# Optimization experiments

Hardware: AMD Instinct MI355X
Metric: run time of the kernel (lower is better)

The kernel has to match this reference:

```python
import jax, jax.numpy as jnp
import numpy as np

BATCH = 32
NUM_PRIORS = 8732
NUM_CLASSES = 81          # includes background class 0
CENTER_VAR = 0.1
SIZE_VAR = 0.2
CONF_THR = 0.01
NMS_THR = 0.45
TOPK = 100                # per-class NMS candidates
MAX_DET = 100             # max detections per image


def setup_inputs() -> dict:
    key = jax.random.key(0)
    k1, k2, k3 = jax.random.split(key, 3)
    cls_logits = jax.random.normal(k1, (BATCH, NUM_PRIORS, NUM_CLASSES), jnp.float32)
    bbox_pred = jax.random.normal(k2, (BATCH, NUM_PRIORS, 4), jnp.float32)
    # center-form priors (cx, cy, w, h) in (0, 1)
    priors = jax.random.uniform(k3, (NUM_PRIORS, 4), jnp.float32, 0.05, 0.95)
    return {"cls_logits": cls_logits, "bbox_pred": bbox_pred, "priors": priors}


def _decode(loc, priors):
    # convert_locations_to_boxes (center form) then center_form_to_corner_form
    cxcy = loc[..., :2] * CENTER_VAR * priors[..., 2:] + priors[..., :2]
    wh = jnp.exp(loc[..., 2:] * SIZE_VAR) * priors[..., 2:]
    return jnp.concatenate([cxcy - wh * 0.5, cxcy + wh * 0.5], axis=-1)  # [.., 4] xyxy


def _pairwise_iou(b):
    # b: [K, 4] corner form
    lt = jnp.maximum(b[:, None, :2], b[None, :, :2])
    rb = jnp.minimum(b[:, None, 2:], b[None, :, 2:])
    wh = jnp.clip(rb - lt, 0.0)
    inter = wh[..., 0] * wh[..., 1]
    area = jnp.clip(b[:, 2] - b[:, 0], 0.0) * jnp.clip(b[:, 3] - b[:, 1], 0.0)
    return inter / (area[:, None] + area[None, :] - inter + 1e-9)


def _per_class_nms(scores_n, boxes_n):
    # scores_n: [N], boxes_n: [N, 4]
    s, idx = jax.lax.top_k(scores_n, TOPK)
    b = boxes_n[idx]                                # [K, 4]
    iou = _pairwise_iou(b)                          # [K, K]
    init = s > CONF_THR
    rng = jnp.arange(TOPK)

    def body(i, keep):
        sup = (iou[i] > NMS_THR) & keep[i] & (rng > i)
        return keep & ~sup

    keep = jax.lax.fori_loop(0, TOPK, body, init)   # greedy NMS on sorted boxes
    return jnp.where(keep, s, 0.0), b


def reference(cls_logits, bbox_pred, priors):
    scores = jax.nn.softmax(cls_logits, axis=-1)            # [B, N, C]
    boxes = _decode(bbox_pred, priors)                      # [B, N, 4]
    cls_scores = jnp.swapaxes(scores[..., 1:], 1, 2)        # [B, C-1, N] skip background
    nms_fn = jax.vmap(jax.vmap(_per_class_nms, in_axes=(0, None)), in_axes=(0, 0))
    s_k, b_k = nms_fn(cls_scores, boxes)                    # [B, C-1, K], [B, C-1, K, 4]
    labels = jnp.broadcast_to(jnp.arange(1, NUM_CLASSES)[None, :, None], s_k.shape)
    B = s_k.shape[0]
    flat = (NUM_CLASSES - 1) * TOPK
    s_f = s_k.reshape(B, flat)
    b_f = b_k.reshape(B, flat, 4)
    l_f = labels.reshape(B, flat)
    top_s, top_i = jax.lax.top_k(s_f, MAX_DET)              # keep best MAX_DET per image
    top_b = jnp.take_along_axis(b_f, top_i[..., None], axis=1)
    top_l = jnp.take_along_axis(l_f, top_i, axis=1)
    return top_b, top_s, top_l.astype(jnp.int32)
```

## Files before the change

### kernel.cpp

```cpp
#include <hip/hip_runtime.h>
#include <hip/hip_bf16.h>
#include <float.h>

#define BATCH    32
#define NPRIORS  8732
#define NT       137
#define NPAD     (NT * 64)
#define NV4T     (NPAD / 4)
#define NCLASSES 81
#define NC1      80
#define TOPK     100
#define MAXDET   100
#define FLATC    (NC1 * TOPK)
#define FV4      2000
#define NCAND    512
#define NBIN     1024
#define BINOFF   3040

__global__ __launch_bounds__(256) void softmax_transpose_kernel(
    const float* __restrict__ logits, float* __restrict__ scores_t) {
  int b = blockIdx.x / NT;
  int tile = blockIdx.x - b * NT;
  int n0 = tile * 64;
  int rows = min(64, NPRIORS - n0);

  int t = threadIdx.x;
  int r = t >> 2;
  int q = t & 3;

  __shared__ __align__(16) float lds[NC1 * 80];

  const bool live = (r < rows);

  float v[21];
  float s = 0.f;
  if (live) {
    const float* rowp = logits + ((size_t)b * NPRIORS + n0 + r) * NCLASSES;
#pragma unroll
    for (int k = 0; k < 20; ++k) v[k] = rowp[q + (k << 2)];
    v[20] = (q == 0) ? rowp[80] : -FLT_MAX;

    float m = -FLT_MAX;
#pragma unroll
    for (int k = 0; k < 20; ++k) m = fmaxf(m, v[k]);
    if (q == 0) m = fmaxf(m, v[20]);
    m = fmaxf(m, __shfl_xor(m, 1));
    m = fmaxf(m, __shfl_xor(m, 2));

#pragma unroll
    for (int k = 0; k < 20; ++k) {
      v[k] = expf(v[k] - m);
      s += v[k];
    }
    if (q == 0) {
      v[20] = expf(v[20] - m);
      s += v[20];
    }
    s += __shfl_xor(s, 1);
    s += __shfl_xor(s, 2);

#pragma unroll
    for (int k = 0; k < 20; ++k) {
      int c = q + (k << 2);
      if (c >= 1) lds[(c - 1) * 80 + r] = v[k] / s;
    }
    if (q == 0) lds[79 * 80 + r] = v[20] / s;
  } else {
#pragma unroll
    for (int k = 0; k < 20; ++k) {
      int c = q + (k << 2);
      if (c >= 1) lds[(c - 1) * 80 + r] = 0.f;
    }
    if (q == 0) lds[79 * 80 + r] = 0.f;
  }
  __syncthreads();

  float4* d4 = (float4*)(scores_t + (size_t)(b * NT + tile) * (NC1 * 64));
#pragma unroll
  for (int i = 0; i < 5; ++i) {
    int o4 = t + (i << 8);
    int c = o4 >> 4;
    int j = o4 & 15;
    d4[o4] = *(const float4*)&lds[c * 80 + (j << 2)];
  }
}

__device__ __forceinline__ float4 decode_box(float4 l, float4 p) {
  float cx = l.x * 0.1f * p.z + p.x;
  float cy = l.y * 0.1f * p.w + p.y;
  float w  = expf(l.z * 0.2f) * p.z;
  float h  = expf(l.w * 0.2f) * p.w;
  return make_float4(cx - w * 0.5f, cy - h * 0.5f, cx + w * 0.5f,
                     cy + h * 0.5f);
}

__device__ __forceinline__ unsigned long long cex(unsigned long long key,
                                                  unsigned long long p,
                                                  bool up, bool low) {
  return (up == low) ? (key < p ? key : p) : (key > p ? key : p);
}

__global__ __launch_bounds__(256, 8) void topk_select_kernel(
    const float* __restrict__ scores_t, unsigned long long* __restrict__ k_sel) {
  const int bc = blockIdx.x;
  const int b = bc / NC1;
  const int c = bc - b * NC1;
  const int t = threadIdx.x;
  const int lane = t & 63;
  const int w = t >> 6;

  __shared__ __align__(16) unsigned int hist[NBIN * 2];
  __shared__ __align__(16) unsigned long long cand[NCAND];
  __shared__ int s_cnt, s_cut, wtot[4];

  const float4* s4 = (const float4*)scores_t;
  const size_t base4 = (size_t)b * (NT * NC1 * 16) + (size_t)c * 16;

  float va[36];
#pragma unroll
  for (int i = 0; i < 9; ++i) {
    int p = t + (i << 8);
    float4 v = make_float4(0.f, 0.f, 0.f, 0.f);
    if (p < NV4T) v = s4[base4 + (size_t)(p >> 4) * (NC1 * 16) + (p & 15)];
    va[4 * i + 0] = v.x; va[4 * i + 1] = v.y;
    va[4 * i + 2] = v.z; va[4 * i + 3] = v.w;
  }
#pragma unroll
  for (int j = 0; j < 36; ++j) asm volatile("" : "+v"(va[j]));

  uint4* h4 = (uint4*)hist;
  const uint4 z4 = make_uint4(0u, 0u, 0u, 0u);
  h4[t] = z4;
  h4[t + 256] = z4;
  cand[t] = ~0ull;
  cand[t + 256] = ~0ull;
  if (t == 0) { s_cnt = 0; s_cut = 0; }
  __syncthreads();

#pragma unroll
  for (int j = 0; j < 36; ++j) {
    unsigned int bits = __float_as_uint(va[j]);
    if (bits != 0u) {
      int bin = (int)(bits >> 18) - BINOFF;
      bin = max(0, min(NBIN - 1, bin));
      atomicAdd(&hist[(bin << 1) | (lane & 1)], 1u);
    }
  }
  __syncthreads();

  int h[4];
  int ls;
  {
    uint4 a = h4[2 * t];
    uint4 b2 = h4[2 * t + 1];
    h[0] = (int)(a.x + a.y);
    h[1] = (int)(a.z + a.w);
    h[2] = (int)(b2.x + b2.y);
    h[3] = (int)(b2.z + b2.w);
    ls = h[0] + h[1] + h[2] + h[3];
  }
  int s = ls;
#pragma unroll
  for (int off = 1; off < 64; off <<= 1) {
    int o = __shfl_down(s, off);
    if (lane + off < 64) s += o;
  }
  if (lane == 0) wtot[w] = s;
  __syncthreads();
  int upper = 0;
  for (int w2 = w + 1; w2 < 4; ++w2) upper += wtot[w2];
  int run = (s - ls) + upper;
  int cutbin = -1;
#pragma unroll
  for (int k = 3; k >= 0; --k) {
    if (run < TOPK && run + h[k] >= TOPK) cutbin = (t << 2) + k;
    run += h[k];
  }
  if (cutbin >= 0) s_cut = cutbin;
  __syncthreads();

  const unsigned int cutbits = (unsigned int)(s_cut + BINOFF) << 18;

  unsigned long long msk = 0ull;
  int cnt = 0;
#pragma unroll
  for (int j = 0; j < 36; ++j) {
    unsigned int bits = __float_as_uint(va[j]);
    if (bits >= cutbits) { msk |= 1ull << j; ++cnt; }
  }
  int inc = cnt;
#pragma unroll
  for (int off = 1; off < 64; off <<= 1) {
    int o = __shfl_up(inc, off);
    if (lane >= off) inc += o;
  }
  int wtotal = __shfl(inc, 63);
  int wbase = 0;
  if (lane == 63) wbase = atomicAdd(&s_cnt, wtotal);
  wbase = __shfl(wbase, 63);
  int pos = wbase + inc - cnt;
#pragma unroll
  for (int j = 0; j < 36; ++j) {
    if ((msk >> j) & 1ull) {
      if (pos < NCAND) {
        unsigned int bits = __float_as_uint(va[j]);
        int idx = ((t + ((j >> 2) << 8)) << 2) + (j & 3);
        cand[pos] = (((unsigned long long)(~bits)) << 32) | (unsigned int)idx;
      }
      ++pos;
    }
  }
  __syncthreads();

  const int ncand = s_cnt;
  if (ncand <= 256) {
    unsigned long long key = cand[t];
#pragma unroll
    for (int k2 = 2; k2 <= 256; k2 <<= 1) {
#pragma unroll
      for (int j = 128; j > 0; j >>= 1) {
        if (j >= k2) continue;
        const bool up = ((t & k2) == 0);
        if (j >= 64) {
          cand[t] = key;
          __syncthreads();
          unsigned long long p = cand[t ^ j];
          key = cex(key, p, up, (t & j) == 0);
          __syncthreads();
        } else {
          unsigned long long p = __shfl_xor(key, j);
          key = cex(key, p, up, (lane & j) == 0);
        }
      }
    }
    if (t < TOPK) k_sel[(size_t)bc * TOPK + t] = key;
  } else {
    int NS = 512;
    for (int k2 = 2; k2 <= NS; k2 <<= 1) {
      for (int j = k2 >> 1; j > 0; j >>= 1) {
        if (j >= 128) {
          __syncthreads();
          for (int p = t; p < NS; p += 256) {
            int ixj = p ^ j;
            if (ixj > p) {
              unsigned long long a = cand[p], c2 = cand[ixj];
              bool up = ((p & k2) == 0);
              if (up ? (a > c2) : (a < c2)) { cand[p] = c2; cand[ixj] = a; }
            }
          }
          __syncthreads();
        } else {
          int base = w << 7;
          if (base < NS) {
#pragma unroll
            for (int half = 0; half < 2; ++half) {
              int p = base + lane + (half << 6);
              int ixj = p ^ j;
              if (ixj > p) {
                unsigned long long a = cand[p], c2 = cand[ixj];
                bool up = ((p & k2) == 0);
                if (up ? (a > c2) : (a < c2)) { cand[p] = c2; cand[ixj] = a; }
              }
            }
          }
        }
      }
    }
    __syncthreads();
    if (t < TOPK) k_sel[(size_t)bc * TOPK + t] = cand[t];
  }
}

__global__ __launch_bounds__(256) void nms_kernel(
    const unsigned long long* __restrict__ k_sel,
    const float* __restrict__ loc, const float* __restrict__ priors,
    float* __restrict__ s_k, float* __restrict__ b_k) {
  const int t = threadIdx.x;
  const int lane = t & 63;
  const int w = t >> 6;
  const int bc = blockIdx.x;
  const int b = bc / NC1;

  __shared__ __align__(16) float4 lbox[TOPK];
  __shared__ float larea[TOPK];
  __shared__ float lscore[TOPK];
  __shared__ unsigned long long pm[4][64][3];
  __shared__ unsigned long long keepw[2];

  if (t < TOPK) {
    unsigned long long key = k_sel[(size_t)bc * TOPK + t];
    float sv = __uint_as_float(~(unsigned int)(key >> 32));
    int idx = (int)(key & 0xFFFFFFFFull);
    if ((unsigned)idx >= NPRIORS) { idx = 0; sv = 0.f; }
    float4 bx = decode_box(((const float4*)loc)[(size_t)b * NPRIORS + idx],
                           ((const float4*)priors)[idx]);
    lbox[t] = bx;
    larea[t] = fmaxf(bx.z - bx.x, 0.f) * fmaxf(bx.w - bx.y, 0.f);
    lscore[t] = sv;
  }
  __syncthreads();

  const bool hasb = (lane + 64) < TOPK;
  float4 ba = lbox[lane];
  float aa = larea[lane];
  float4 bb2 = lbox[hasb ? (lane + 64) : 0];
  float ab = larea[hasb ? (lane + 64) : 0];

  unsigned long long ra0 = 0, ra1 = 0, rb1 = 0;
  int jlo = max(1, w * 25);
  int jhi = min(TOPK, w * 25 + 25);
  for (int j = jlo; j < jhi; ++j) {
    float4 bj = lbox[j];
    float aj = larea[j];
    if (lane < j) {
      float iw = fmaxf(fminf(ba.z, bj.z) - fmaxf(ba.x, bj.x), 0.f);
      float ih = fmaxf(fminf(ba.w, bj.w) - fmaxf(ba.y, bj.y), 0.f);
      float inter = iw * ih;
      float iou = inter / (aa + aj - inter + 1e-9f);
      if (iou > 0.45f) {
        if (j < 64) ra0 |= 1ull << j; else ra1 |= 1ull << (j - 64);
      }
    }
    if (hasb && (lane + 64) < j) {
      float iw = fmaxf(fminf(bb2.z, bj.z) - fmaxf(bb2.x, bj.x), 0.f);
      float ih = fmaxf(fminf(bb2.w, bj.w) - fmaxf(bb2.y, bj.y), 0.f);
      float inter = iw * ih;
      float iou = inter / (ab + aj - inter + 1e-9f);
      if (iou > 0.45f) rb1 |= 1ull << (j - 64);
    }
  }
  pm[w][lane][0] = ra0;
  pm[w][lane][1] = ra1;
  pm[w][lane][2] = rb1;
  __syncthreads();

  if (w == 0) {
    unsigned long long fa0 = pm[0][lane][0] | pm[1][lane][0] |
                             pm[2][lane][0] | pm[3][lane][0];
    unsigned long long fa1 = pm[0][lane][1] | pm[1][lane][1] |
                             pm[2][lane][1] | pm[3][lane][1];
    unsigned long long fb1 = pm[0][lane][2] | pm[1][lane][2] |
                             pm[2][lane][2] | pm[3][lane][2];

    float sva = lscore[lane];
    float svb = hasb ? lscore[lane + 64] : 0.f;
    unsigned long long keep0 = __ballot(sva > 0.01f);
    unsigned long long keep1 = __ballot(hasb && (svb > 0.01f));
    for (int i = 0; i < TOPK; ++i) {
      bool il = i < 64;
      bool kb = il ? ((keep0 >> i) & 1ull) : ((keep1 >> (i - 64)) & 1ull);
      unsigned long long m0 = __shfl(il ? fa0 : 0ull, i & 63);
      unsigned long long m1 = __shfl(il ? fa1 : fb1, i & 63);
      if (kb) { keep0 &= ~m0; keep1 &= ~m1; }
    }
    if (lane == 0) { keepw[0] = keep0; keepw[1] = keep1; }
  }
  __syncthreads();

  if (t < TOPK) {
    bool kp = (t < 64) ? ((keepw[0] >> t) & 1ull)
                       : ((keepw[1] >> (t - 64)) & 1ull);
    s_k[(size_t)bc * TOPK + t] = kp ? lscore[t] : 0.f;
    ((float4*)(b_k + (size_t)bc * TOPK * 4))[t] = lbox[t];
  }
}

__global__ __launch_bounds__(256) void final_topk_kernel(
    const float* __restrict__ s_k, const float* __restrict__ b_k,
    float* __restrict__ out) {
  const int b = blockIdx.x;
  const int t = threadIdx.x;
  const int lane = t & 63;
  const int w = t >> 6;

  __shared__ __align__(16) unsigned int hist[NBIN * 2];
  __shared__ __align__(16) unsigned long long cand[NCAND];
  __shared__ int s_cnt, s_cut, wtot[4];

  const float4* src4 = (const float4*)(s_k + (size_t)b * FLATC);

  float va[32];
#pragma unroll
  for (int i = 0; i < 8; ++i) {
    int p = t + (i << 8);
    float4 v = make_float4(0.f, 0.f, 0.f, 0.f);
    if (p < FV4) v = src4[p];
    va[4 * i + 0] = v.x; va[4 * i + 1] = v.y;
    va[4 * i + 2] = v.z; va[4 * i + 3] = v.w;
  }

  uint4* h4 = (uint4*)hist;
  const uint4 z4 = make_uint4(0u, 0u, 0u, 0u);
  h4[t] = z4;
  h4[t + 256] = z4;
  cand[t] = ~0ull;
  cand[t + 256] = ~0ull;
  if (t == 0) { s_cnt = 0; s_cut = 0; }
  __syncthreads();

#pragma unroll
  for (int j = 0; j < 32; ++j) {
    unsigned int bits = __float_as_uint(va[j]);
    if (bits != 0u) {
      int bin = (int)(bits >> 18) - BINOFF;
      bin = max(0, min(NBIN - 1, bin));
      atomicAdd(&hist[(bin << 1) | (lane & 1)], 1u);
    }
  }
  __syncthreads();

  int h[4];
  int ls;
  {
    uint4 a = h4[2 * t];
    uint4 b2 = h4[2 * t + 1];
    h[0] = (int)(a.x + a.y);
    h[1] = (int)(a.z + a.w);
    h[2] = (int)(b2.x + b2.y);
    h[3] = (int)(b2.z + b2.w);
    ls = h[0] + h[1] + h[2] + h[3];
  }
  int s = ls;
#pragma unroll
  for (int off = 1; off < 64; off <<= 1) {
    int o = __shfl_down(s, off);
    if (lane + off < 64) s += o;
  }
  if (lane == 0) wtot[w] = s;
  __syncthreads();
  int upper = 0;
  for (int w2 = w + 1; w2 < 4; ++w2) upper += wtot[w2];
  int run = (s - ls) + upper;
  int cutbin = -1;
#pragma unroll
  for (int k = 3; k >= 0; --k) {
    if (run < TOPK && run + h[k] >= TOPK) cutbin = (t << 2) + k;
    run += h[k];
  }
  if (cutbin >= 0) s_cut = cutbin;
  __syncthreads();

  const unsigned int cutbits = (unsigned int)(s_cut + BINOFF) << 18;

  unsigned int msk = 0u;
  int cnt = 0;
#pragma unroll
  for (int j = 0; j < 32; ++j) {
    unsigned int bits = __float_as_uint(va[j]);
    if (bits >= cutbits) { msk |= 1u << j; ++cnt; }
  }
  int inc = cnt;
#pragma unroll
  for (int off = 1; off < 64; off <<= 1) {
    int o = __shfl_up(inc, off);
    if (lane >= off) inc += o;
  }
  int wtotal = __shfl(inc, 63);
  int wbase = 0;
  if (lane == 63) wbase = atomicAdd(&s_cnt, wtotal);
  wbase = __shfl(wbase, 63);
  int pos = wbase + inc - cnt;
#pragma unroll
  for (int j = 0; j < 32; ++j) {
    if ((msk >> j) & 1u) {
      if (pos < NCAND) {
        unsigned int bits = __float_as_uint(va[j]);
        int idx = ((t + ((j >> 2) << 8)) << 2) + (j & 3);
        cand[pos] = (((unsigned long long)(~bits)) << 32) | (unsigned int)idx;
      }
      ++pos;
    }
  }
  __syncthreads();

  const int ncand = s_cnt;
  unsigned long long okey;
  if (ncand <= 256) {
    unsigned long long key = cand[t];
#pragma unroll
    for (int k2 = 2; k2 <= 256; k2 <<= 1) {
#pragma unroll
      for (int j = 128; j > 0; j >>= 1) {
        if (j >= k2) continue;
        const bool up = ((t & k2) == 0);
        if (j >= 64) {
          cand[t] = key;
          __syncthreads();
          unsigned long long p = cand[t ^ j];
          key = cex(key, p, up, (t & j) == 0);
          __syncthreads();
        } else {
          unsigned long long p = __shfl_xor(key, j);
          key = cex(key, p, up, (lane & j) == 0);
        }
      }
    }
    okey = key;
  } else {
    int NS = 512;
    for (int k2 = 2; k2 <= NS; k2 <<= 1) {
      for (int j = k2 >> 1; j > 0; j >>= 1) {
        if (j >= 128) {
          __syncthreads();
          for (int p = t; p < NS; p += 256) {
            int ixj = p ^ j;
            if (ixj > p) {
              unsigned long long a = cand[p], c2 = cand[ixj];
              bool up = ((p & k2) == 0);
              if (up ? (a > c2) : (a < c2)) { cand[p] = c2; cand[ixj] = a; }
            }
          }
          __syncthreads();
        } else {
          int base = w << 7;
          if (base < NS) {
#pragma unroll
            for (int half = 0; half < 2; ++half) {
              int p = base + lane + (half << 6);
              int ixj = p ^ j;
              if (ixj > p) {
                unsigned long long a = cand[p], c2 = cand[ixj];
                bool up = ((p & k2) == 0);
                if (up ? (a > c2) : (a < c2)) { cand[p] = c2; cand[ixj] = a; }
              }
            }
          }
        }
      }
    }
    __syncthreads();
    okey = cand[min(t, NCAND - 1)];
  }

  if (t < MAXDET) {
    unsigned long long key = okey;
    unsigned int vb = ~(unsigned int)(key >> 32);
    float sv = __uint_as_float(vb);
    int f = (int)(key & 0xFFFFFFFFull);
    if ((unsigned)f >= FLATC) { f = 0; sv = 0.f; }
    float4 bb = *(const float4*)(b_k + ((size_t)b * FLATC + f) * 4);
    ((float4*)out)[b * MAXDET + t] = bb;
    out[BATCH * MAXDET * 4 + b * MAXDET + t] = sv;
    int cls = f / TOPK + 1;
    out[BATCH * MAXDET * 5 + b * MAXDET + t] = (float)cls;
  }
}

extern "C" void kernel_launch(void* const* d_in, const int* in_sizes, int n_in,
                              void* d_out, int out_size, void* d_ws,
                              size_t ws_size, hipStream_t stream) {
  const float* cls_logits = (const float*)d_in[0];
  const float* bbox_pred  = (const float*)d_in[1];
  const float* priors     = (const float*)d_in[2];
  float* out = (float*)d_out;

  float* scores_t = (float*)d_ws;
  float* s_k = scores_t + (size_t)BATCH * NT * NC1 * 64;
  float* b_k = s_k + (size_t)BATCH * NC1 * TOPK;
  unsigned long long* k_sel =
      (unsigned long long*)(b_k + (size_t)BATCH * NC1 * TOPK * 4);

  softmax_transpose_kernel<<<BATCH * NT, 256, 0, stream>>>(cls_logits,
                                                           scores_t);
  topk_select_kernel<<<BATCH * NC1, 256, 0, stream>>>(scores_t, k_sel);
  nms_kernel<<<BATCH * NC1, 256, 0, stream>>>(k_sel, bbox_pred, priors,
                                              s_k, b_k);
  final_topk_kernel<<<BATCH, 256, 0, stream>>>(s_k, b_k, out);
}
```

Before: 104.5 us.

## Fuse per-class top-k selection and NMS into one kernel

Merges the top-k selection kernel and the NMS kernel into a single kernel. The selected keys now stay in shared memory instead of passing through a global buffer, and the NMS buffers reuse the histogram and candidate shared arrays. This removes one kernel launch and a global write and read of the 100 keys per class. The fused kernel keeps launch_bounds(256,8), so register pressure from the NMS part could lower occupancy or cause spills in the selection phase.

```diff
diff --git a/kernel.cpp b/kernel.cpp
--- a/kernel.cpp
+++ b/kernel.cpp
@@ -100,8 +100,10 @@
   return (up == low) ? (key < p ? key : p) : (key > p ? key : p);
 }
 
-__global__ __launch_bounds__(256, 8) void topk_select_kernel(
-    const float* __restrict__ scores_t, unsigned long long* __restrict__ k_sel) {
+__global__ __launch_bounds__(256, 8) void topk_nms_kernel(
+    const float* __restrict__ scores_t, const float* __restrict__ loc,
+    const float* __restrict__ priors, float* __restrict__ s_k,
+    float* __restrict__ b_k) {
   const int bc = blockIdx.x;
   const int b = bc / NC1;
   const int c = bc - b * NC1;
@@ -111,6 +113,7 @@
 
   __shared__ __align__(16) unsigned int hist[NBIN * 2];
   __shared__ __align__(16) unsigned long long cand[NCAND];
+  __shared__ __align__(16) unsigned long long skey[TOPK];
   __shared__ int s_cnt, s_cut, wtot[4];
 
   const float4* s4 = (const float4*)scores_t;
@@ -233,7 +236,7 @@
         }
       }
     }
-    if (t < TOPK) k_sel[(size_t)bc * TOPK + t] = key;
+    if (t < TOPK) skey[t] = key;
   } else {
     int NS = 512;
     for (int k2 = 2; k2 <= NS; k2 <<= 1) {
@@ -267,30 +270,21 @@
       }
     }
     __syncthreads();
-    if (t < TOPK) k_sel[(size_t)bc * TOPK + t] = cand[t];
-  }
-}
-
-__global__ __launch_bounds__(256) void nms_kernel(
-    const unsigned long long* __restrict__ k_sel,
-    const float* __restrict__ loc, const float* __restrict__ priors,
-    float* __restrict__ s_k, float* __restrict__ b_k) {
-  const int t = threadIdx.x;
-  const int lane = t & 63;
-  const int w = t >> 6;
-  const int bc = blockIdx.x;
-  const int b = bc / NC1;
-
-  __shared__ __align__(16) float4 lbox[TOPK];
-  __shared__ float larea[TOPK];
-  __shared__ float lscore[TOPK];
-  __shared__ unsigned long long pm[4][64][3];
-  __shared__ unsigned long long keepw[2];
+    if (t < TOPK) skey[t] = cand[t];
+  }
+  __syncthreads();
+
+  typedef unsigned long long ull;
+  float4* lbox  = (float4*)cand;
+  float*  larea = (float*)((char*)cand + 1600);
+  float*  lscore= (float*)((char*)cand + 2000);
+  ull*    pmbuf = (ull*)hist;
+  ull*    keepw = (ull*)((char*)hist + 6144);
 
   if (t < TOPK) {
-    unsigned long long key = k_sel[(size_t)bc * TOPK + t];
-    float sv = __uint_as_float(~(unsigned int)(key >> 32));
-    int idx = (int)(key & 0xFFFFFFFFull);
+    ull key2 = skey[t];
+    float sv = __uint_as_float(~(unsigned int)(key2 >> 32));
+    int idx = (int)(key2 & 0xFFFFFFFFull);
     if ((unsigned)idx >= NPRIORS) { idx = 0; sv = 0.f; }
     float4 bx = decode_box(((const float4*)loc)[(size_t)b * NPRIORS + idx],
                            ((const float4*)priors)[idx]);
@@ -306,7 +300,7 @@
   float4 bb2 = lbox[hasb ? (lane + 64) : 0];
   float ab = larea[hasb ? (lane + 64) : 0];
 
-  unsigned long long ra0 = 0, ra1 = 0, rb1 = 0;
+  ull ra0 = 0, ra1 = 0, rb1 = 0;
   int jlo = max(1, w * 25);
   int jhi = min(TOPK, w * 25 + 25);
   for (int j = jlo; j < jhi; ++j) {
@@ -329,28 +323,28 @@
       if (iou > 0.45f) rb1 |= 1ull << (j - 64);
     }
   }
-  pm[w][lane][0] = ra0;
-  pm[w][lane][1] = ra1;
-  pm[w][lane][2] = rb1;
+  pmbuf[((w << 6) + lane) * 3 + 0] = ra0;
+  pmbuf[((w << 6) + lane) * 3 + 1] = ra1;
+  pmbuf[((w << 6) + lane) * 3 + 2] = rb1;
   __syncthreads();
 
   if (w == 0) {
-    unsigned long long fa0 = pm[0][lane][0] | pm[1][lane][0] |
-                             pm[2][lane][0] | pm[3][lane][0];
-    unsigned long long fa1 = pm[0][lane][1] | pm[1][lane][1] |
-                             pm[2][lane][1] | pm[3][lane][1];
-    unsigned long long fb1 = pm[0][lane][2] | pm[1][lane][2] |
-                             pm[2][lane][2] | pm[3][lane][2];
+    ull fa0 = pmbuf[lane * 3 + 0] | pmbuf[(64 + lane) * 3 + 0] |
+              pmbuf[(128 + lane) * 3 + 0] | pmbuf[(192 + lane) * 3 + 0];
+    ull fa1 = pmbuf[lane * 3 + 1] | pmbuf[(64 + lane) * 3 + 1] |
+              pmbuf[(128 + lane) * 3 + 1] | pmbuf[(192 + lane) * 3 + 1];
+    ull fb1 = pmbuf[lane * 3 + 2] | pmbuf[(64 + lane) * 3 + 2] |
+              pmbuf[(128 + lane) * 3 + 2] | pmbuf[(192 + lane) * 3 + 2];
 
     float sva = lscore[lane];
     float svb = hasb ? lscore[lane + 64] : 0.f;
-    unsigned long long keep0 = __ballot(sva > 0.01f);
-    unsigned long long keep1 = __ballot(hasb && (svb > 0.01f));
+    ull keep0 = __ballot(sva > 0.01f);
+    ull keep1 = __ballot(hasb && (svb > 0.01f));
     for (int i = 0; i < TOPK; ++i) {
       bool il = i < 64;
       bool kb = il ? ((keep0 >> i) & 1ull) : ((keep1 >> (i - 64)) & 1ull);
-      unsigned long long m0 = __shfl(il ? fa0 : 0ull, i & 63);
-      unsigned long long m1 = __shfl(il ? fa1 : fb1, i & 63);
+      ull m0 = __shfl(il ? fa0 : 0ull, i & 63);
+      ull m1 = __shfl(il ? fa1 : fb1, i & 63);
       if (kb) { keep0 &= ~m0; keep1 &= ~m1; }
     }
     if (lane == 0) { keepw[0] = keep0; keepw[1] = keep1; }
@@ -557,13 +551,10 @@
   float* scores_t = (float*)d_ws;
   float* s_k = scores_t + (size_t)BATCH * NT * NC1 * 64;
   float* b_k = s_k + (size_t)BATCH * NC1 * TOPK;
-  unsigned long long* k_sel =
-      (unsigned long long*)(b_k + (size_t)BATCH * NC1 * TOPK * 4);
 
   softmax_transpose_kernel<<<BATCH * NT, 256, 0, stream>>>(cls_logits,
                                                            scores_t);
-  topk_select_kernel<<<BATCH * NC1, 256, 0, stream>>>(scores_t, k_sel);
-  nms_kernel<<<BATCH * NC1, 256, 0, stream>>>(k_sel, bbox_pred, priors,
-                                              s_k, b_k);
+  topk_nms_kernel<<<BATCH * NC1, 256, 0, stream>>>(scores_t, bbox_pred,
+                                                   priors, s_k, b_k);
   final_topk_kernel<<<BATCH, 256, 0, stream>>>(s_k, b_k, out);
 }
```

Result: faster. 100.8 us (median of 2 runs) (-3.5%).
